# Kernel optimization log

Measured on AMD Instinct MI355X. Metric: run time of the kernel, lower is better.

## Reference

```python
import jax, jax.numpy as jnp
import numpy as np

NUM_HEADS = 16

def setup_inputs() -> dict:
    key = jax.random.key(0)
    ks = jax.random.split(key, 6)
    C = 512
    nW, B, N = 64, 4, 144
    x = jax.random.normal(ks[0], (B * nW, N, C), dtype=jnp.float32)
    mask = jax.random.randint(ks[1], (nW, N, N), 0, 2, dtype=jnp.int32)
    Wqkv = jax.random.normal(ks[2], (C, 3 * C), dtype=jnp.float32) * (1.0 / np.sqrt(C))
    bqkv = jnp.zeros((3 * C,), dtype=jnp.float32)
    Wproj = jax.random.normal(ks[3], (C, C), dtype=jnp.float32) * (1.0 / np.sqrt(C))
    bproj = jnp.zeros((C,), dtype=jnp.float32)
    return {"x": x, "mask": mask, "Wqkv": Wqkv, "bqkv": bqkv, "Wproj": Wproj, "bproj": bproj}

def reference(x, mask, Wqkv, bqkv, Wproj, bproj):
    Bn, N, C = x.shape
    H = NUM_HEADS
    D = C // H
    nW = mask.shape[0]
    B = Bn // nW
    scale = 1.0 / jnp.sqrt(jnp.asarray(D, dtype=x.dtype))

    qkv = x @ Wqkv + bqkv                        # (Bn, N, 3C)
    qkv = qkv.reshape(Bn, N, 3, H, D)            # packed order (qkv, H, D)
    qkv = jnp.transpose(qkv, (2, 0, 3, 1, 4))    # (3, Bn, H, N, D)
    q, k, v = qkv[0], qkv[1], qkv[2]

    # split window-batch dim: (B nW) -> B, nW
    q = q.reshape(B, nW, H, N, D)
    k = k.reshape(B, nW, H, N, D)
    v = v.reshape(B, nW, H, N, D)

    attn = jnp.einsum('bwhnd,bwhmd->bwhnm', q, k) * scale
    bias = jnp.where(mask == 0, -jnp.inf, 0.0).astype(x.dtype)  # (nW, N, N)
    attn = attn + bias.reshape(1, nW, 1, N, N)
    attn = jax.nn.softmax(attn, axis=-1)

    out = jnp.einsum('bwhnm,bwhmd->bwhnd', attn, v)   # (B, nW, H, N, D)
    out = jnp.transpose(out, (0, 1, 3, 2, 4)).reshape(Bn, N, C)
    return out @ Wproj + bproj
```

## Files before the change

kernel.cpp:

```cpp
#include <hip/hip_runtime.h>

typedef unsigned short u16;
typedef unsigned int u32;
typedef __attribute__((ext_vector_type(4))) float f32x4;
typedef __attribute__((ext_vector_type(8))) short bf16x8;
typedef __attribute__((ext_vector_type(4))) u32 u32x4;

__device__ __forceinline__ u16 f2bf(float f) {
  union { float f; u32 u; } v; v.f = f;
  u32 r = v.u + 0x7fffu + ((v.u >> 16) & 1u);
  return (u16)(r >> 16);
}

__device__ __forceinline__ void gload_lds16(const u16* g, u16* l) {
  __builtin_amdgcn_global_load_lds((__attribute__((address_space(1))) const void*)g,
                                   (__attribute__((address_space(3))) void*)l,
                                   16, 0, 0);
}

__global__ void __launch_bounds__(256) k_transpose_w(const float* __restrict__ W,
                                                     u16* __restrict__ Wt, int K, int Nc) {
  __shared__ u16 t[64][72];
  const int tid = threadIdx.x;
  const int kb = blockIdx.x * 64, nb = blockIdx.y * 64;
  const int c4 = (tid & 15) * 4;
  const int r0 = tid >> 4;
#pragma unroll
  for (int rr = 0; rr < 4; ++rr) {
    int r = rr * 16 + r0;
    float4 v = *(const float4*)(W + (size_t)(kb + r) * Nc + nb + c4);
    t[r][c4 + 0] = f2bf(v.x);
    t[r][c4 + 1] = f2bf(v.y);
    t[r][c4 + 2] = f2bf(v.z);
    t[r][c4 + 3] = f2bf(v.w);
  }
  __syncthreads();
  const int c8 = (tid & 7) * 8;
  const int rn = tid >> 3;
#pragma unroll
  for (int rr = 0; rr < 2; ++rr) {
    int n = rr * 32 + rn;
    u16 tmp[8];
#pragma unroll
    for (int j = 0; j < 8; ++j) tmp[j] = t[c8 + j][n];
    *(u32x4*)(Wt + (size_t)(nb + n) * K + kb + c8) = *(const u32x4*)tmp;
  }
}

__global__ void k_mask_bits(const int* __restrict__ mask, u32* __restrict__ mtab) {
  int idx = blockIdx.x * blockDim.x + threadIdx.x;
  if (idx >= 64 * 144 * 8) return;
  int wd = idx & 7;
  int r = idx >> 3;
  u32 bits = 0;
  if (wd < 5) {
    int base = r * 144 + wd * 32;
    int nmax = 144 - wd * 32;
    if (nmax > 32) nmax = 32;
    for (int b = 0; b < nmax; ++b) bits |= (mask[base + b] ? 1u : 0u) << b;
  }
  mtab[idx] = bits;
}

template <bool OUT_BF16, bool A_FP32>
__global__ void __launch_bounds__(256, 3) k_gemm(const void* __restrict__ Ap,
                                                 const u16* __restrict__ Bt,
                                                 const float* __restrict__ bias,
                                                 void* __restrict__ D,
                                                 int Nc, int K, int NB) {
  __shared__ u16 As[128 * 68];
  __shared__ u16 Bs[2][128 * 64];
  const int tid = threadIdx.x;
  const int wave = tid >> 6, lane = tid & 63;
  const int wr = wave >> 1, wc = wave & 1;
  const int l15 = lane & 15, g = lane >> 4;
  const int sx = l15 & 7;
  const f32x4 fzero = {0.f, 0.f, 0.f, 0.f};

  const int cpx = gridDim.x >> 3;
  const int swz = (blockIdx.x & 7) * cpx + (blockIdx.x >> 3);
  const int bm = swz / NB, bn = swz % NB;

  const u16* Bb = Bt + (size_t)bn * 128 * K;

  int rr[4], cc[4];
#pragma unroll
  for (int i = 0; i < 4; ++i) {
    int e = i * 256 + tid;
    rr[i] = e >> 3;
    cc[i] = e & 7;
  }

  f32x4 acc[4][4];
#pragma unroll
  for (int m = 0; m < 4; ++m)
#pragma unroll
    for (int n = 0; n < 4; ++n) acc[m][n] = fzero;

  f32x4 areg[8];
  u32x4 aregb[4];

  auto A_LOAD = [&](int ks) {
    if constexpr (A_FP32) {
      const float* Af = (const float*)Ap;
#pragma unroll
      for (int i = 0; i < 4; ++i) {
        const float* p = Af + (size_t)(bm * 128 + rr[i]) * K + ks + cc[i] * 8;
        areg[2 * i] = *(const f32x4*)(p);
        areg[2 * i + 1] = *(const f32x4*)(p + 4);
      }
    } else {
      const u16* Ab = (const u16*)Ap + (size_t)bm * 128 * K;
#pragma unroll
      for (int i = 0; i < 4; ++i)
        aregb[i] = *(const u32x4*)(Ab + (size_t)rr[i] * K + ks + cc[i] * 8);
    }
  };

  auto A_WRITE = [&]() {
#pragma unroll
    for (int i = 0; i < 4; ++i) {
      u32x4 wv;
      if constexpr (A_FP32) {
        u32 w0, w1, w2, w3;
        asm("v_cvt_pk_bf16_f32 %0, %1, %2" : "=v"(w0) : "v"(areg[2 * i][0]), "v"(areg[2 * i][1]));
        asm("v_cvt_pk_bf16_f32 %0, %1, %2" : "=v"(w1) : "v"(areg[2 * i][2]), "v"(areg[2 * i][3]));
        asm("v_cvt_pk_bf16_f32 %0, %1, %2" : "=v"(w2) : "v"(areg[2 * i + 1][0]), "v"(areg[2 * i + 1][1]));
        asm("v_cvt_pk_bf16_f32 %0, %1, %2" : "=v"(w3) : "v"(areg[2 * i + 1][2]), "v"(areg[2 * i + 1][3]));
        wv[0] = w0; wv[1] = w1; wv[2] = w2; wv[3] = w3;
      } else {
        wv = aregb[i];
      }
      *(u32x4*)(&As[rr[i] * 68 + cc[i] * 8]) = wv;
    }
  };

  auto B_STAGE = [&](int buf, int ks) {
#pragma unroll
    for (int i = 0; i < 4; ++i) {
      int cs = cc[i] ^ (rr[i] & 7);
      gload_lds16(Bb + (size_t)rr[i] * K + ks + (cs << 3), &Bs[buf][(i * 256 + tid) * 8]);
    }
  };

  auto COMPUTE = [&](int buf) {
#pragma unroll
    for (int kk = 0; kk < 2; ++kk) {
      bf16x8 a[4], b[4];
#pragma unroll
      for (int m = 0; m < 4; ++m)
        a[m] = *(const bf16x8*)(&As[(wr * 64 + m * 16 + l15) * 68 + (kk * 4 + g) * 8]);
#pragma unroll
      for (int n = 0; n < 4; ++n)
        b[n] = *(const bf16x8*)(&Bs[buf][(wc * 64 + n * 16 + l15) * 64 + (((kk * 4 + g) ^ sx) << 3)]);
#pragma unroll
      for (int m = 0; m < 4; ++m)
#pragma unroll
        for (int n = 0; n < 4; ++n)
          acc[m][n] = __builtin_amdgcn_mfma_f32_16x16x32_bf16(a[m], b[n], acc[m][n], 0, 0, 0);
    }
  };

  const int nt = K >> 6;
  A_LOAD(0);
  B_STAGE(0, 0);
  int cur = 0;
  for (int t = 0; t < nt; ++t) {
    asm volatile("s_waitcnt vmcnt(0)" ::: "memory");
    __builtin_amdgcn_sched_barrier(0);
    if (t + 1 < nt) B_STAGE(cur ^ 1, (t + 1) << 6);
    A_WRITE();
    if (t + 1 < nt) A_LOAD((t + 1) << 6);
    asm volatile("s_waitcnt lgkmcnt(0)" ::: "memory");
    __builtin_amdgcn_sched_barrier(0);
    __builtin_amdgcn_s_barrier();
    __builtin_amdgcn_sched_barrier(0);
    COMPUTE(cur);
    __builtin_amdgcn_sched_barrier(0);
    if (t + 1 < nt) __builtin_amdgcn_s_barrier();
    cur ^= 1;
  }

  const int row0 = bm * 128 + wr * 64;
  const int col0 = bn * 128 + wc * 64;
#pragma unroll
  for (int m = 0; m < 4; ++m) {
#pragma unroll
    for (int n = 0; n < 4; ++n) {
      int col = col0 + n * 16 + l15;
      float bv = bias[col];
#pragma unroll
      for (int j = 0; j < 4; ++j) {
        int row = row0 + m * 16 + g * 4 + j;
        float v = acc[m][n][j] + bv;
        if constexpr (OUT_BF16)
          ((u16*)D)[(size_t)row * Nc + col] = f2bf(v);
        else
          ((float*)D)[(size_t)row * Nc + col] = v;
      }
    }
  }
}

__global__ void __launch_bounds__(256) k_attn(const u16* __restrict__ qkv,
                                              const u32* __restrict__ mtab,
                                              u16* __restrict__ obuf) {
  __shared__ u16 k_s[144 * 40];
  __shared__ u16 vT_s[32 * 168];
  __shared__ u16 P_s[4][16 * 168];

  const int bh = blockIdx.x;
  const int bn = bh >> 4, h = bh & 15;
  const int wid = bn & 63;
  const int tid = threadIdx.x;
  const int wave = tid >> 6, lane = tid & 63;
  const int l15 = lane & 15, g = lane >> 4;
  const f32x4 fzero = {0.f, 0.f, 0.f, 0.f};

  const u16* base = qkv + (size_t)bn * 144 * 1536 + h * 32;

  for (int e = tid; e < 576; e += 256) {
    int n = e >> 2, c = e & 3;
    const u16* rowp = base + (size_t)n * 1536 + c * 8;
    u32x4 kv = *(const u32x4*)(rowp + 512);
    u32x4 vv = *(const u32x4*)(rowp + 1024);
    *(u32x4*)(k_s + n * 40 + c * 8) = kv;
#pragma unroll
    for (int t = 0; t < 4; ++t) {
      u32 w = vv[t];
      vT_s[(c * 8 + 2 * t) * 168 + n] = (u16)(w & 0xffffu);
      vT_s[(c * 8 + 2 * t + 1) * 168 + n] = (u16)(w >> 16);
    }
  }
  for (int e = tid; e < 512; e += 256) {
    int d = e >> 4, c = e & 15;
    vT_s[d * 168 + 144 + c] = 0;
  }
  __syncthreads();

  const float scale = 0.17677669529663687f;
  u16* Pw = &P_s[wave][0];

  for (int mt = wave; mt < 9; mt += 4) {
    u32 mw[4][5];
#pragma unroll
    for (int j = 0; j < 4; ++j) {
      int r = mt * 16 + g * 4 + j;
      const u32* mp = mtab + ((size_t)(wid * 144 + r) << 3);
#pragma unroll
      for (int wd = 0; wd < 5; ++wd) mw[j][wd] = mp[wd];
    }

    bf16x8 a = *(const bf16x8*)(base + (size_t)(mt * 16 + l15) * 1536 + g * 8);

    f32x4 accs[9];
#pragma unroll
    for (int nt = 0; nt < 9; ++nt) {
      bf16x8 b = *(const bf16x8*)(k_s + (nt * 16 + l15) * 40 + g * 8);
      accs[nt] = __builtin_amdgcn_mfma_f32_16x16x32_bf16(a, b, fzero, 0, 0, 0);
    }

    float rmax[4] = {-1e30f, -1e30f, -1e30f, -1e30f};
#pragma unroll
    for (int nt = 0; nt < 9; ++nt) {
      const int wd = nt >> 1;
      const int sh = (nt & 1) * 16;
#pragma unroll
      for (int j = 0; j < 4; ++j) {
        float x = accs[nt][j] * scale;
        u32 bit = (mw[j][wd] >> (sh + l15)) & 1u;
        x = bit ? x : -1e9f;
        accs[nt][j] = x;
        rmax[j] = fmaxf(rmax[j], x);
      }
    }
#pragma unroll
    for (int off = 1; off < 16; off <<= 1)
#pragma unroll
      for (int j = 0; j < 4; ++j)
        rmax[j] = fmaxf(rmax[j], __shfl_xor(rmax[j], off, 64));

    float rsum[4] = {0.f, 0.f, 0.f, 0.f};
#pragma unroll
    for (int nt = 0; nt < 9; ++nt)
#pragma unroll
      for (int j = 0; j < 4; ++j) {
        float p = __expf(accs[nt][j] - rmax[j]);
        accs[nt][j] = p;
        rsum[j] += p;
      }
#pragma unroll
    for (int off = 1; off < 16; off <<= 1)
#pragma unroll
      for (int j = 0; j < 4; ++j)
        rsum[j] += __shfl_xor(rsum[j], off, 64);
    float rinv[4];
#pragma unroll
    for (int j = 0; j < 4; ++j) rinv[j] = 1.f / rsum[j];

#pragma unroll
    for (int nt = 0; nt < 9; ++nt)
#pragma unroll
      for (int j = 0; j < 4; ++j)
        Pw[(g * 4 + j) * 168 + nt * 16 + l15] = f2bf(accs[nt][j] * rinv[j]);
#pragma unroll
    for (int j = 0; j < 4; ++j)
      Pw[(g * 4 + j) * 168 + 144 + l15] = 0;

    asm volatile("s_waitcnt lgkmcnt(0)" ::: "memory");
    __builtin_amdgcn_sched_barrier(0);

    f32x4 acco[2];
    acco[0] = fzero;
    acco[1] = fzero;
#pragma unroll
    for (int kk = 0; kk < 5; ++kk) {
      bf16x8 pa = *(const bf16x8*)(Pw + l15 * 168 + kk * 32 + g * 8);
#pragma unroll
      for (int nt2 = 0; nt2 < 2; ++nt2) {
        bf16x8 b = *(const bf16x8*)(vT_s + (nt2 * 16 + l15) * 168 + kk * 32 + g * 8);
        acco[nt2] = __builtin_amdgcn_mfma_f32_16x16x32_bf16(pa, b, acco[nt2], 0, 0, 0);
      }
    }
#pragma unroll
    for (int nt2 = 0; nt2 < 2; ++nt2)
#pragma unroll
      for (int j = 0; j < 4; ++j) {
        int r = mt * 16 + g * 4 + j;
        int d = nt2 * 16 + l15;
        obuf[((size_t)bn * 144 + r) * 512 + h * 32 + d] = f2bf(acco[nt2][j]);
      }
  }
}

extern "C" void kernel_launch(void* const* d_in, const int* in_sizes, int n_in,
                              void* d_out, int out_size, void* d_ws, size_t ws_size,
                              hipStream_t stream) {
  const float* x = (const float*)d_in[0];
  const int* mask = (const int*)d_in[1];
  const float* Wqkv = (const float*)d_in[2];
  const float* bqkv = (const float*)d_in[3];
  const float* Wproj = (const float*)d_in[4];
  const float* bproj = (const float*)d_in[5];
  float* out = (float*)d_out;

  char* ws = (char*)d_ws;
  u32* mtab    = (u32*)(ws + 0);
  u16* wqkv_t  = (u16*)(ws + 294912);
  u16* qkv     = (u16*)(ws + 1867776);
  u16* obuf    = (u16*)(ws + 115113984);
  u16* wproj_t = (u16*)(ws + 152862720);

  k_transpose_w<<<dim3(8, 24), 256, 0, stream>>>(Wqkv, wqkv_t, 512, 1536);
  k_transpose_w<<<dim3(8, 8), 256, 0, stream>>>(Wproj, wproj_t, 512, 512);
  k_mask_bits<<<288, 256, 0, stream>>>(mask, mtab);
  k_gemm<true, true><<<3456, 256, 0, stream>>>(x, wqkv_t, bqkv, qkv, 1536, 512, 12);
  k_attn<<<4096, 256, 0, stream>>>(qkv, mtab, obuf);
  k_gemm<false, false><<<1152, 256, 0, stream>>>(obuf, wproj_t, bproj, out, 512, 512, 4);
}
```

Measured before the change: 220.6 us.

## Add dedicated 256x256-tile QKV GEMM with double-buffered LDS and interleaved loads

Replaces the generic QKV projection GEMM with a dedicated kernel that uses 512 threads and 256x256 output tiles. Both A and B are double-buffered in LDS with an XOR swizzle, and the next tile's loads are staged in phases between MFMA groups, using explicit waitcnt, barriers and setprio. The larger tiles are meant to cut global reloads of x and the weights and to hide memory latency behind compute. The cost is more LDS and registers per block (lower occupancy) and fewer blocks, which risks underfilling CUs. The output-projection GEMM is simplified to a bf16-only A path.

```diff
diff --git a/kernel.cpp b/kernel.cpp
--- a/kernel.cpp
+++ b/kernel.cpp
@@ -62,8 +62,147 @@
   mtab[idx] = bits;
 }
 
-template <bool OUT_BF16, bool A_FP32>
-__global__ void __launch_bounds__(256, 3) k_gemm(const void* __restrict__ Ap,
+__global__ void __launch_bounds__(512) k_gemm1(const float* __restrict__ A,
+                                               const u16* __restrict__ Bt,
+                                               const float* __restrict__ bias,
+                                               u16* __restrict__ D,
+                                               int Nc, int K, int NB) {
+  __shared__ u16 As[2][256 * 64];
+  __shared__ u16 Bs[2][256 * 64];
+  const int tid = threadIdx.x;
+  const int wave = tid >> 6, lane = tid & 63;
+  const int wr = wave >> 2, wc = wave & 3;
+  const int l15 = lane & 15, g = lane >> 4;
+  const int sx = l15 & 7;
+  const f32x4 fzero = {0.f, 0.f, 0.f, 0.f};
+
+  const int cpx = gridDim.x >> 3;
+  const int swz = (blockIdx.x & 7) * cpx + (blockIdx.x >> 3);
+  const int bm = swz / NB, bn = swz % NB;
+
+  const u16* Bb = Bt + (size_t)bn * 256 * K;
+
+  f32x4 acc[8][4];
+#pragma unroll
+  for (int m = 0; m < 8; ++m)
+#pragma unroll
+    for (int n = 0; n < 4; ++n) acc[m][n] = fzero;
+
+  f32x4 areg[8];
+
+  auto A_LOAD = [&](int tt) {
+#pragma unroll
+    for (int i = 0; i < 4; ++i) {
+      int e = i * 512 + tid;
+      int r = e >> 3, c = e & 7;
+      const float* p = A + (size_t)(bm * 256 + r) * K + (tt << 6) + c * 8;
+      areg[2 * i] = *(const f32x4*)(p);
+      areg[2 * i + 1] = *(const f32x4*)(p + 4);
+    }
+  };
+
+  auto A_WRITE = [&](int buf) {
+#pragma unroll
+    for (int i = 0; i < 4; ++i) {
+      int e = i * 512 + tid;
+      int r = e >> 3, c = e & 7;
+      u32 w0, w1, w2, w3;
+      asm("v_cvt_pk_bf16_f32 %0, %1, %2" : "=v"(w0) : "v"(areg[2 * i][0]), "v"(areg[2 * i][1]));
+      asm("v_cvt_pk_bf16_f32 %0, %1, %2" : "=v"(w1) : "v"(areg[2 * i][2]), "v"(areg[2 * i][3]));
+      asm("v_cvt_pk_bf16_f32 %0, %1, %2" : "=v"(w2) : "v"(areg[2 * i + 1][0]), "v"(areg[2 * i + 1][1]));
+      asm("v_cvt_pk_bf16_f32 %0, %1, %2" : "=v"(w3) : "v"(areg[2 * i + 1][2]), "v"(areg[2 * i + 1][3]));
+      u32x4 wv = {w0, w1, w2, w3};
+      *(u32x4*)(&As[buf][r * 64 + ((c ^ (r & 7)) << 3)]) = wv;
+    }
+  };
+
+  auto B_HALF = [&](int buf, int h, int tt) {
+#pragma unroll
+    for (int i = 0; i < 2; ++i) {
+      int e = h * 1024 + i * 512 + tid;
+      int r = e >> 3, c = e & 7;
+      gload_lds16(Bb + (size_t)r * K + (tt << 6) + ((c ^ (r & 7)) << 3), &Bs[buf][e * 8]);
+    }
+  };
+
+  const int nt = K >> 6;
+
+  A_LOAD(0);
+  B_HALF(0, 0, 0);
+  B_HALF(0, 1, 0);
+  asm volatile("s_waitcnt vmcnt(4)" ::: "memory");
+  __builtin_amdgcn_sched_barrier(0);
+  A_WRITE(0);
+  asm volatile("s_waitcnt lgkmcnt(0)" ::: "memory");
+  __builtin_amdgcn_sched_barrier(0);
+  __builtin_amdgcn_s_barrier();
+
+  for (int t = 0; t < nt; ++t) {
+    const int cur = t & 1;
+    const bool more = (t + 1 < nt);
+#pragma unroll
+    for (int p = 0; p < 4; ++p) {
+      const int mh = p & 1, kk = p >> 1;
+      if (p == 0) {
+        if (more) {
+          A_LOAD(t + 1);
+          B_HALF(cur ^ 1, 0, t + 1);
+          asm volatile("s_waitcnt vmcnt(10)" ::: "memory");
+        } else {
+          asm volatile("s_waitcnt vmcnt(0)" ::: "memory");
+        }
+        __builtin_amdgcn_sched_barrier(0);
+        __builtin_amdgcn_s_barrier();
+      }
+      const int cx = ((kk * 4 + g) ^ sx) << 3;
+      bf16x8 a[4], b[4];
+#pragma unroll
+      for (int m = 0; m < 4; ++m)
+        a[m] = *(const bf16x8*)(&As[cur][(wr * 128 + mh * 64 + m * 16 + l15) * 64 + cx]);
+#pragma unroll
+      for (int n = 0; n < 4; ++n)
+        b[n] = *(const bf16x8*)(&Bs[cur][(wc * 64 + n * 16 + l15) * 64 + cx]);
+      if (p == 1 && more) B_HALF(cur ^ 1, 1, t + 1);
+      if (p == 3 && more) {
+        asm volatile("s_waitcnt vmcnt(4)" ::: "memory");
+        __builtin_amdgcn_sched_barrier(0);
+        A_WRITE(cur ^ 1);
+      }
+      if (p != 0) __builtin_amdgcn_s_barrier();
+      asm volatile("s_waitcnt lgkmcnt(0)" ::: "memory");
+      __builtin_amdgcn_sched_barrier(0);
+      __builtin_amdgcn_s_setprio(1);
+#pragma unroll
+      for (int m = 0; m < 4; ++m)
+#pragma unroll
+        for (int n = 0; n < 4; ++n)
+          acc[mh * 4 + m][n] =
+              __builtin_amdgcn_mfma_f32_16x16x32_bf16(a[m], b[n], acc[mh * 4 + m][n], 0, 0, 0);
+      __builtin_amdgcn_s_setprio(0);
+      __builtin_amdgcn_sched_barrier(0);
+      __builtin_amdgcn_s_barrier();
+    }
+  }
+
+  const int row0 = bm * 256 + wr * 128;
+  const int col0 = bn * 256 + wc * 64;
+#pragma unroll
+  for (int m = 0; m < 8; ++m) {
+#pragma unroll
+    for (int n = 0; n < 4; ++n) {
+      int col = col0 + n * 16 + l15;
+      float bv = bias[col];
+#pragma unroll
+      for (int j = 0; j < 4; ++j) {
+        int row = row0 + m * 16 + g * 4 + j;
+        D[(size_t)row * Nc + col] = f2bf(acc[m][n][j] + bv);
+      }
+    }
+  }
+}
+
+template <bool OUT_BF16>
+__global__ void __launch_bounds__(256, 3) k_gemm(const u16* __restrict__ Ab,
                                                  const u16* __restrict__ Bt,
                                                  const float* __restrict__ bias,
                                                  void* __restrict__ D,
@@ -81,6 +220,7 @@
   const int swz = (blockIdx.x & 7) * cpx + (blockIdx.x >> 3);
   const int bm = swz / NB, bn = swz % NB;
 
+  const u16* Ap = Ab + (size_t)bm * 128 * K;
   const u16* Bb = Bt + (size_t)bn * 128 * K;
 
   int rr[4], cc[4];
@@ -97,44 +237,18 @@
 #pragma unroll
     for (int n = 0; n < 4; ++n) acc[m][n] = fzero;
 
-  f32x4 areg[8];
   u32x4 aregb[4];
 
   auto A_LOAD = [&](int ks) {
-    if constexpr (A_FP32) {
-      const float* Af = (const float*)Ap;
-#pragma unroll
-      for (int i = 0; i < 4; ++i) {
-        const float* p = Af + (size_t)(bm * 128 + rr[i]) * K + ks + cc[i] * 8;
-        areg[2 * i] = *(const f32x4*)(p);
-        areg[2 * i + 1] = *(const f32x4*)(p + 4);
-      }
-    } else {
-      const u16* Ab = (const u16*)Ap + (size_t)bm * 128 * K;
-#pragma unroll
-      for (int i = 0; i < 4; ++i)
-        aregb[i] = *(const u32x4*)(Ab + (size_t)rr[i] * K + ks + cc[i] * 8);
-    }
-  };
-
+#pragma unroll
+    for (int i = 0; i < 4; ++i)
+      aregb[i] = *(const u32x4*)(Ap + (size_t)rr[i] * K + ks + cc[i] * 8);
+  };
   auto A_WRITE = [&]() {
 #pragma unroll
-    for (int i = 0; i < 4; ++i) {
-      u32x4 wv;
-      if constexpr (A_FP32) {
-        u32 w0, w1, w2, w3;
-        asm("v_cvt_pk_bf16_f32 %0, %1, %2" : "=v"(w0) : "v"(areg[2 * i][0]), "v"(areg[2 * i][1]));
-        asm("v_cvt_pk_bf16_f32 %0, %1, %2" : "=v"(w1) : "v"(areg[2 * i][2]), "v"(areg[2 * i][3]));
-        asm("v_cvt_pk_bf16_f32 %0, %1, %2" : "=v"(w2) : "v"(areg[2 * i + 1][0]), "v"(areg[2 * i + 1][1]));
-        asm("v_cvt_pk_bf16_f32 %0, %1, %2" : "=v"(w3) : "v"(areg[2 * i + 1][2]), "v"(areg[2 * i + 1][3]));
-        wv[0] = w0; wv[1] = w1; wv[2] = w2; wv[3] = w3;
-      } else {
-        wv = aregb[i];
-      }
-      *(u32x4*)(&As[rr[i] * 68 + cc[i] * 8]) = wv;
-    }
-  };
-
+    for (int i = 0; i < 4; ++i)
+      *(u32x4*)(&As[rr[i] * 68 + cc[i] * 8]) = aregb[i];
+  };
   auto B_STAGE = [&](int buf, int ks) {
 #pragma unroll
     for (int i = 0; i < 4; ++i) {
@@ -142,7 +256,6 @@
       gload_lds16(Bb + (size_t)rr[i] * K + ks + (cs << 3), &Bs[buf][(i * 256 + tid) * 8]);
     }
   };
-
   auto COMPUTE = [&](int buf) {
 #pragma unroll
     for (int kk = 0; kk < 2; ++kk) {
@@ -354,7 +467,7 @@
   k_transpose_w<<<dim3(8, 24), 256, 0, stream>>>(Wqkv, wqkv_t, 512, 1536);
   k_transpose_w<<<dim3(8, 8), 256, 0, stream>>>(Wproj, wproj_t, 512, 512);
   k_mask_bits<<<288, 256, 0, stream>>>(mask, mtab);
-  k_gemm<true, true><<<3456, 256, 0, stream>>>(x, wqkv_t, bqkv, qkv, 1536, 512, 12);
+  k_gemm1<<<864, 512, 0, stream>>>(x, wqkv_t, bqkv, qkv, 1536, 512, 6);
   k_attn<<<4096, 256, 0, stream>>>(qkv, mtab, obuf);
-  k_gemm<false, false><<<1152, 256, 0, stream>>>(obuf, wproj_t, bproj, out, 512, 512, 4);
-}
+  k_gemm<false><<<1152, 256, 0, stream>>>(obuf, wproj_t, bproj, out, 512, 512, 4);
+}
```

After: 242.3 us. 1.1x slower.

## Transpose QK MFMA so softmax rows live per lane, use three waves

Applied to the files above, without the earlier changes.

The attention kernel now computes S^T by swapping MFMA operands (K as A, Q as B), so each lane holds one query row across its accumulator entries. This reduces the row max/sum reductions from 4-step shuffles over 4 rows to two shuffles of one value, and loads mask words once per lane. P is written with packed bf16 conversion as 32-bit stores. The block shrinks from 4 to 3 waves so 9 row tiles split evenly (3 each), which raises per-wave work and may reduce occupancy per block.

```diff
diff --git a/kernel.cpp b/kernel.cpp
--- a/kernel.cpp
+++ b/kernel.cpp
@@ -202,12 +202,12 @@
   }
 }
 
-__global__ void __launch_bounds__(256) k_attn(const u16* __restrict__ qkv,
+__global__ void __launch_bounds__(192) k_attn(const u16* __restrict__ qkv,
                                               const u32* __restrict__ mtab,
                                               u16* __restrict__ obuf) {
   __shared__ u16 k_s[144 * 40];
   __shared__ u16 vT_s[32 * 168];
-  __shared__ u16 P_s[4][16 * 168];
+  __shared__ u16 P_s[3][16 * 168];
 
   const int bh = blockIdx.x;
   const int bn = bh >> 4, h = bh & 15;
@@ -219,7 +219,7 @@
 
   const u16* base = qkv + (size_t)bn * 144 * 1536 + h * 32;
 
-  for (int e = tid; e < 576; e += 256) {
+  for (int e = tid; e < 576; e += 192) {
     int n = e >> 2, c = e & 3;
     const u16* rowp = base + (size_t)n * 1536 + c * 8;
     u32x4 kv = *(const u32x4*)(rowp + 512);
@@ -232,7 +232,7 @@
       vT_s[(c * 8 + 2 * t + 1) * 168 + n] = (u16)(w >> 16);
     }
   }
-  for (int e = tid; e < 512; e += 256) {
+  for (int e = tid; e < 512; e += 192) {
     int d = e >> 4, c = e & 15;
     vT_s[d * 168 + 144 + c] = 0;
   }
@@ -241,71 +241,63 @@
   const float scale = 0.17677669529663687f;
   u16* Pw = &P_s[wave][0];
 
-  for (int mt = wave; mt < 9; mt += 4) {
-    u32 mw[4][5];
-#pragma unroll
-    for (int j = 0; j < 4; ++j) {
-      int r = mt * 16 + g * 4 + j;
-      const u32* mp = mtab + ((size_t)(wid * 144 + r) << 3);
-#pragma unroll
-      for (int wd = 0; wd < 5; ++wd) mw[j][wd] = mp[wd];
-    }
-
-    bf16x8 a = *(const bf16x8*)(base + (size_t)(mt * 16 + l15) * 1536 + g * 8);
+  for (int mt = wave; mt < 9; mt += 3) {
+    bf16x8 qb = *(const bf16x8*)(base + (size_t)(mt * 16 + l15) * 1536 + g * 8);
+
+    const u32* mp = mtab + ((size_t)(wid * 144 + mt * 16 + l15) << 3);
+    u32 mw[5];
+#pragma unroll
+    for (int wd = 0; wd < 5; ++wd) mw[wd] = mp[wd];
 
     f32x4 accs[9];
 #pragma unroll
     for (int nt = 0; nt < 9; ++nt) {
-      bf16x8 b = *(const bf16x8*)(k_s + (nt * 16 + l15) * 40 + g * 8);
-      accs[nt] = __builtin_amdgcn_mfma_f32_16x16x32_bf16(a, b, fzero, 0, 0, 0);
-    }
-
-    float rmax[4] = {-1e30f, -1e30f, -1e30f, -1e30f};
+      bf16x8 kf = *(const bf16x8*)(k_s + (nt * 16 + l15) * 40 + g * 8);
+      accs[nt] = __builtin_amdgcn_mfma_f32_16x16x32_bf16(kf, qb, fzero, 0, 0, 0);
+    }
+
+    float rmax = -1e30f;
 #pragma unroll
     for (int nt = 0; nt < 9; ++nt) {
       const int wd = nt >> 1;
-      const int sh = (nt & 1) * 16;
+      const int shb = (nt & 1) * 16;
 #pragma unroll
       for (int j = 0; j < 4; ++j) {
         float x = accs[nt][j] * scale;
-        u32 bit = (mw[j][wd] >> (sh + l15)) & 1u;
+        u32 bit = (mw[wd] >> (shb + g * 4 + j)) & 1u;
         x = bit ? x : -1e9f;
         accs[nt][j] = x;
-        rmax[j] = fmaxf(rmax[j], x);
-      }
-    }
-#pragma unroll
-    for (int off = 1; off < 16; off <<= 1)
-#pragma unroll
-      for (int j = 0; j < 4; ++j)
-        rmax[j] = fmaxf(rmax[j], __shfl_xor(rmax[j], off, 64));
-
-    float rsum[4] = {0.f, 0.f, 0.f, 0.f};
+        rmax = fmaxf(rmax, x);
+      }
+    }
+    rmax = fmaxf(rmax, __shfl_xor(rmax, 16, 64));
+    rmax = fmaxf(rmax, __shfl_xor(rmax, 32, 64));
+
+    float rsum = 0.f;
 #pragma unroll
     for (int nt = 0; nt < 9; ++nt)
 #pragma unroll
       for (int j = 0; j < 4; ++j) {
-        float p = __expf(accs[nt][j] - rmax[j]);
+        float p = __expf(accs[nt][j] - rmax);
         accs[nt][j] = p;
-        rsum[j] += p;
-      }
-#pragma unroll
-    for (int off = 1; off < 16; off <<= 1)
-#pragma unroll
-      for (int j = 0; j < 4; ++j)
-        rsum[j] += __shfl_xor(rsum[j], off, 64);
-    float rinv[4];
-#pragma unroll
-    for (int j = 0; j < 4; ++j) rinv[j] = 1.f / rsum[j];
-
-#pragma unroll
-    for (int nt = 0; nt < 9; ++nt)
-#pragma unroll
-      for (int j = 0; j < 4; ++j)
-        Pw[(g * 4 + j) * 168 + nt * 16 + l15] = f2bf(accs[nt][j] * rinv[j]);
-#pragma unroll
-    for (int j = 0; j < 4; ++j)
-      Pw[(g * 4 + j) * 168 + 144 + l15] = 0;
+        rsum += p;
+      }
+    rsum += __shfl_xor(rsum, 16, 64);
+    rsum += __shfl_xor(rsum, 32, 64);
+    const float rinv = 1.f / rsum;
+
+#pragma unroll
+    for (int nt = 0; nt < 9; ++nt) {
+      u32 w0, w1;
+      float p0 = accs[nt][0] * rinv, p1 = accs[nt][1] * rinv;
+      float p2 = accs[nt][2] * rinv, p3 = accs[nt][3] * rinv;
+      asm("v_cvt_pk_bf16_f32 %0, %1, %2" : "=v"(w0) : "v"(p0), "v"(p1));
+      asm("v_cvt_pk_bf16_f32 %0, %1, %2" : "=v"(w1) : "v"(p2), "v"(p3));
+      *(u32*)(Pw + l15 * 168 + nt * 16 + g * 4) = w0;
+      *(u32*)(Pw + l15 * 168 + nt * 16 + g * 4 + 2) = w1;
+    }
+    *(u32*)(Pw + l15 * 168 + 144 + g * 4) = 0;
+    *(u32*)(Pw + l15 * 168 + 144 + g * 4 + 2) = 0;
 
     asm volatile("s_waitcnt lgkmcnt(0)" ::: "memory");
     __builtin_amdgcn_sched_barrier(0);
@@ -355,6 +347,6 @@
   k_transpose_w<<<dim3(8, 8), 256, 0, stream>>>(Wproj, wproj_t, 512, 512);
   k_mask_bits<<<288, 256, 0, stream>>>(mask, mtab);
   k_gemm<true, true><<<3456, 256, 0, stream>>>(x, wqkv_t, bqkv, qkv, 1536, 512, 12);
-  k_attn<<<4096, 256, 0, stream>>>(qkv, mtab, obuf);
+  k_attn<<<4096, 192, 0, stream>>>(qkv, mtab, obuf);
   k_gemm<false, false><<<1152, 256, 0, stream>>>(obuf, wproj_t, bproj, out, 512, 512, 4);
 }
```

New measurement: 204.1 us. 1.08x faster.
